# Kernel optimization log

Hardware: AMD Instinct MI355X
Metric: run time of the kernel (lower is better)

The kernel has to match this reference:

```python
import jax, jax.numpy as jnp
import numpy as np
from jax import lax

KS = 3          # kernel_size
ITER = 24       # diffusion iterations
# itertools.product([0,1,-1], repeat=2) order from the torch source
OFFS = [(i, j) for i in (0, 1, -1) for j in (0, 1, -1)]


def setup_inputs() -> dict:
    key = jax.random.key(0)
    k1, k2, k3 = jax.random.split(key, 3)
    B, H, W = 8, 512, 512
    x = jax.random.normal(k1, (B, 1, H, W), jnp.float32)
    W_aff = jax.random.normal(k2, (KS * KS - 1, 1, KS, KS), jnp.float32) * 0.1
    b_aff = jax.random.normal(k3, (KS * KS - 1,), jnp.float32) * 0.1
    return {"x": x, "W_aff": W_aff, "b_aff": b_aff}


def _gen_kernel(aff):
    # aff: [B, 8, H, W] -> normalized 9-channel kernel [B, 9, H, W]
    abs_sum = jnp.sum(jnp.abs(aff), axis=1, keepdims=True)
    a = aff / abs_sum
    s = jnp.sum(a, axis=1, keepdims=True)
    return jnp.concatenate([1.0 - s, a], axis=1)


def reference(x, W_aff, b_aff):
    # affinity net: 1 -> 8 channel 3x3 SAME conv
    aff = lax.conv_general_dilated(x, W_aff, (1, 1), "SAME") + b_aff[None, :, None, None]
    kernel = _gen_kernel(aff)  # [B, 9, H, W]
    H, W = x.shape[2], x.shape[3]

    def body(_, xc):
        # zero-pad then take 9 shifted views: col_k[p] = x[p - off_k] (zero outside)
        xp = jnp.pad(xc, ((0, 0), (0, 0), (1, 1), (1, 1)))
        cols = jnp.concatenate(
            [xp[:, :, 1 - oi:1 - oi + H, 1 - oj:1 - oj + W] for (oi, oj) in OFFS],
            axis=1,
        )  # [B, 9, H, W]
        return jnp.sum(cols * kernel, axis=1, keepdims=True)

    return lax.fori_loop(0, ITER, body, x)
```

## Files before the change

### kernel.cpp

```cpp
#include <hip/hip_runtime.h>
#include <hip/hip_fp16.h>

constexpr int B = 8, H = 512, W = 512;
constexpr int N = B * H * W;
constexpr int HW = H * W;

constexpr int TT = 32;
constexpr int T  = 6;
constexpr int XR = TT + 2 * T;
constexpr int XE = XR * XR;
constexpr int NG = XR / 4;
constexpr int CR = XR - 2;
constexpr int NGT = CR * NG;
constexpr int NTH = H / TT, NTW = W / TT;
constexpr int NTILES = B * NTH * NTW;
constexpr int NT = 512;
constexpr int NF2 = XR * (XR / 2);

__global__ __launch_bounds__(256) void cspn_gen_kernel(
    const float* __restrict__ x, const float* __restrict__ Wa,
    const float* __restrict__ ba, __half* __restrict__ Kh) {
  int idx = blockIdx.x * 256 + threadIdx.x;
  if (idx >= N) return;
  int j = idx & (W - 1);
  int i = (idx >> 9) & (H - 1);
  const float* xb = x + (idx & ~(HW - 1));

  float v[9];
#pragma unroll
  for (int u = 0; u < 3; ++u) {
#pragma unroll
    for (int t = 0; t < 3; ++t) {
      int ii = i + u - 1, jj = j + t - 1;
      v[u * 3 + t] = (unsigned(ii) < (unsigned)H && unsigned(jj) < (unsigned)W)
                         ? xb[ii * W + jj]
                         : 0.0f;
    }
  }

  float aff[8];
  float abs_sum = 0.0f;
#pragma unroll
  for (int c = 0; c < 8; ++c) {
    float a = ba[c];
#pragma unroll
    for (int t = 0; t < 9; ++t) a += v[t] * Wa[c * 9 + t];
    aff[c] = a;
    abs_sum += fabsf(a);
  }
  float inv = 1.0f / abs_sum;
#pragma unroll
  for (int c = 0; c < 8; ++c) aff[c] *= inv;

  union { uint4 u; __half2 h[4]; } pk;
#pragma unroll
  for (int c = 0; c < 4; ++c)
    pk.h[c] = __floats2half2_rn(aff[2 * c], aff[2 * c + 1]);
  *reinterpret_cast<uint4*>(Kh + (size_t)idx * 8) = pk.u;
}

#define H2F(h) __half2float(h)

__global__ __launch_bounds__(NT, 6) void cspn_fused(
    const float* __restrict__ xin, const __half* __restrict__ Kh,
    float* __restrict__ xout) {
  __shared__ __align__(16) float sBuf[64 + 2 * XE + 64];
  float* sX = sBuf + 64;

  int bid = blockIdx.x;
  int wg = (bid & 7) * (NTILES / 8) + (bid >> 3);
  int b  = wg / (NTH * NTW);
  int rr = wg % (NTH * NTW);
  int ti0 = (rr / NTW) * TT, tj0 = (rr % NTW) * TT;
  int tid = threadIdx.x;

  bool active = tid < NGT;
  int xi  = 1 + tid / NG;
  int xj0 = (tid % NG) * 4;

  const float* xb = xin + (size_t)b * HW;

  int li0 = tid / (XR / 2), gc0 = tid - li0 * (XR / 2);
  int p1 = tid + NT;
  int li1 = p1 / (XR / 2), gc1 = p1 - li1 * (XR / 2);
  bool st1 = p1 < NF2;
  float2 sv0 = make_float2(0.f, 0.f), sv1 = make_float2(0.f, 0.f);
  {
    int gi = ti0 + li0 - T, gj = tj0 + 2 * gc0 - T;
    if ((unsigned)gi < (unsigned)H && (unsigned)gj < (unsigned)W)
      sv0 = *reinterpret_cast<const float2*>(xb + gi * W + gj);
  }
  if (st1) {
    int gi = ti0 + li1 - T, gj = tj0 + 2 * gc1 - T;
    if ((unsigned)gi < (unsigned)H && (unsigned)gj < (unsigned)W)
      sv1 = *reinterpret_cast<const float2*>(xb + gi * W + gj);
  }

  __half2 kh[4][4];
  float4 k0;
  {
    int gi  = ti0 + xi - T;
    int gj0 = tj0 + xj0 - T;
    bool rowv = active && (unsigned)gi < (unsigned)H;
    const __half* Kb =
        Kh + ((size_t)b * HW + (size_t)(rowv ? gi : 0) * W) * 8;
    float k0v[4];
#pragma unroll
    for (int p = 0; p < 4; ++p) {
      int gj = gj0 + p;
      union { uint4 u; __half2 h[4]; } pk;
      pk.u = make_uint4(0u, 0u, 0u, 0u);
      if (rowv && (unsigned)gj < (unsigned)W)
        pk.u = *reinterpret_cast<const uint4*>(Kb + (size_t)gj * 8);
      float2 f01 = __half22float2(pk.h[0]);
      float2 f23 = __half22float2(pk.h[1]);
      float2 f45 = __half22float2(pk.h[2]);
      float2 f67 = __half22float2(pk.h[3]);
      k0v[p] = 1.0f - (f01.x + f01.y + f23.x + f23.y +
                       f45.x + f45.y + f67.x + f67.y);
      kh[p][0] = pk.h[0]; kh[p][1] = pk.h[1];
      kh[p][2] = pk.h[2]; kh[p][3] = pk.h[3];
    }
    k0 = make_float4(k0v[0], k0v[1], k0v[2], k0v[3]);
  }

  *reinterpret_cast<float2*>(sX + li0 * XR + 2 * gc0) = sv0;
  if (st1) *reinterpret_cast<float2*>(sX + li1 * XR + 2 * gc1) = sv1;
  if (tid < 64) {
    sBuf[tid] = 0.f;
    sBuf[64 + 2 * XE + tid] = 0.f;
  }
  if (tid < 2 * XR) {
    int r = (tid < XR) ? 0 : (XR - 1);
    int c = (tid < XR) ? tid : tid - XR;
    sX[XE + r * XR + c] = 0.f;
  }
  __syncthreads();

  int base = xi * XR + xj0;
  float4 c1;
  if (active) c1 = *reinterpret_cast<const float4*>(sX + base);
#pragma unroll
  for (int s = 0; s < T; ++s) {
    const float* Xc = sX + (s & 1) * XE;
    float* Xn = sX + (((s & 1) ^ 1)) * XE;
    if (active) {
      const float* eu = Xc + base - XR - 1;
      const float* ec = Xc + base - 1;
      const float* ed = Xc + base + XR - 1;
      float l0 = eu[0], r0 = eu[5];
      float l1 = ec[0], r1 = ec[5];
      float l2 = ed[0], r2 = ed[5];
      float4 c0 = *reinterpret_cast<const float4*>(eu + 1);
      float4 c2 = *reinterpret_cast<const float4*>(ed + 1);
      float4 acc;
      acc.x = k0.x * c1.x
            + H2F(kh[0][0].x) * l1   + H2F(kh[0][0].y) * c1.y
            + H2F(kh[0][1].x) * c0.x + H2F(kh[0][1].y) * l0
            + H2F(kh[0][2].x) * c0.y + H2F(kh[0][2].y) * c2.x
            + H2F(kh[0][3].x) * l2   + H2F(kh[0][3].y) * c2.y;
      acc.y = k0.y * c1.y
            + H2F(kh[1][0].x) * c1.x + H2F(kh[1][0].y) * c1.z
            + H2F(kh[1][1].x) * c0.y + H2F(kh[1][1].y) * c0.x
            + H2F(kh[1][2].x) * c0.z + H2F(kh[1][2].y) * c2.y
            + H2F(kh[1][3].x) * c2.x + H2F(kh[1][3].y) * c2.z;
      acc.z = k0.z * c1.z
            + H2F(kh[2][0].x) * c1.y + H2F(kh[2][0].y) * c1.w
            + H2F(kh[2][1].x) * c0.z + H2F(kh[2][1].y) * c0.y
            + H2F(kh[2][2].x) * c0.w + H2F(kh[2][2].y) * c2.z
            + H2F(kh[2][3].x) * c2.y + H2F(kh[2][3].y) * c2.w;
      acc.w = k0.w * c1.w
            + H2F(kh[3][0].x) * c1.z + H2F(kh[3][0].y) * r1
            + H2F(kh[3][1].x) * c0.w + H2F(kh[3][1].y) * c0.z
            + H2F(kh[3][2].x) * r0   + H2F(kh[3][2].y) * c2.w
            + H2F(kh[3][3].x) * c2.z + H2F(kh[3][3].y) * r2;
      *reinterpret_cast<float4*>(Xn + base) = acc;
      c1 = acc;
    }
    __syncthreads();
  }

  float* yb = xout + (size_t)b * HW;
  int i  = tid >> 4;
  int pj = (tid & 15) * 2;
  float2 v = *reinterpret_cast<const float2*>(sX + (i + T) * XR + (pj + T));
  *reinterpret_cast<float2*>(yb + (size_t)(ti0 + i) * W + (tj0 + pj)) = v;
}

extern "C" void kernel_launch(void* const* d_in, const int* in_sizes, int n_in,
                              void* d_out, int out_size, void* d_ws,
                              size_t ws_size, hipStream_t stream) {
  const float* x  = (const float*)d_in[0];
  const float* Wa = (const float*)d_in[1];
  const float* ba = (const float*)d_in[2];
  float* out = (float*)d_out;

  __half* Kh = (__half*)d_ws;
  float* xa = (float*)d_ws + 4 * (size_t)N;
  cspn_gen_kernel<<<dim3(N / 256), dim3(256), 0, stream>>>(x, Wa, ba, Kh);

  const float* src = x;
  for (int l = 0; l < 24 / T; ++l) {
    float* dst = (l & 1) ? out : xa;
    cspn_fused<<<dim3(NTILES), dim3(NT), 0, stream>>>(src, Kh, dst);
    src = dst;
  }
}
```

Baseline: 115.0 us.

## Fuse affinity kernel generation into diffusion kernel, recomputing per launch

Removes the separate kernel-generation pass and its fp16 workspace buffer. Each diffusion launch now recomputes the 3x3 affinity conv and normalization from the original input for its tile, keeping all 9 weights in fp32 registers. This trades the global write and re-read of the packed half kernel for redundant compute in each of the four launches. It also raises register pressure under the existing launch bounds, and the per-thread scalar global loads of x0 are uncoalesced.

```diff
diff --git a/kernel.cpp b/kernel.cpp
--- a/kernel.cpp
+++ b/kernel.cpp
@@ -1,5 +1,4 @@
 #include <hip/hip_runtime.h>
-#include <hip/hip_fp16.h>
 
 constexpr int B = 8, H = 512, W = 512;
 constexpr int N = B * H * W;
@@ -17,52 +16,9 @@
 constexpr int NT = 512;
 constexpr int NF2 = XR * (XR / 2);
 
-__global__ __launch_bounds__(256) void cspn_gen_kernel(
-    const float* __restrict__ x, const float* __restrict__ Wa,
-    const float* __restrict__ ba, __half* __restrict__ Kh) {
-  int idx = blockIdx.x * 256 + threadIdx.x;
-  if (idx >= N) return;
-  int j = idx & (W - 1);
-  int i = (idx >> 9) & (H - 1);
-  const float* xb = x + (idx & ~(HW - 1));
-
-  float v[9];
-#pragma unroll
-  for (int u = 0; u < 3; ++u) {
-#pragma unroll
-    for (int t = 0; t < 3; ++t) {
-      int ii = i + u - 1, jj = j + t - 1;
-      v[u * 3 + t] = (unsigned(ii) < (unsigned)H && unsigned(jj) < (unsigned)W)
-                         ? xb[ii * W + jj]
-                         : 0.0f;
-    }
-  }
-
-  float aff[8];
-  float abs_sum = 0.0f;
-#pragma unroll
-  for (int c = 0; c < 8; ++c) {
-    float a = ba[c];
-#pragma unroll
-    for (int t = 0; t < 9; ++t) a += v[t] * Wa[c * 9 + t];
-    aff[c] = a;
-    abs_sum += fabsf(a);
-  }
-  float inv = 1.0f / abs_sum;
-#pragma unroll
-  for (int c = 0; c < 8; ++c) aff[c] *= inv;
-
-  union { uint4 u; __half2 h[4]; } pk;
-#pragma unroll
-  for (int c = 0; c < 4; ++c)
-    pk.h[c] = __floats2half2_rn(aff[2 * c], aff[2 * c + 1]);
-  *reinterpret_cast<uint4*>(Kh + (size_t)idx * 8) = pk.u;
-}
-
-#define H2F(h) __half2float(h)
-
 __global__ __launch_bounds__(NT, 6) void cspn_fused(
-    const float* __restrict__ xin, const __half* __restrict__ Kh,
+    const float* __restrict__ x0, const float* __restrict__ Wa,
+    const float* __restrict__ ba, const float* __restrict__ xin,
     float* __restrict__ xout) {
   __shared__ __align__(16) float sBuf[64 + 2 * XE + 64];
   float* sX = sBuf + 64;
@@ -78,7 +34,8 @@
   int xi  = 1 + tid / NG;
   int xj0 = (tid % NG) * 4;
 
-  const float* xb = xin + (size_t)b * HW;
+  const float* xb  = xin + (size_t)b * HW;
+  const float* x0b = x0 + (size_t)b * HW;
 
   int li0 = tid / (XR / 2), gc0 = tid - li0 * (XR / 2);
   int p1 = tid + NT;
@@ -96,32 +53,49 @@
       sv1 = *reinterpret_cast<const float2*>(xb + gi * W + gj);
   }
 
-  __half2 kh[4][4];
-  float4 k0;
-  {
+  float kkv[9][4];
+  if (active) {
     int gi  = ti0 + xi - T;
     int gj0 = tj0 + xj0 - T;
-    bool rowv = active && (unsigned)gi < (unsigned)H;
-    const __half* Kb =
-        Kh + ((size_t)b * HW + (size_t)(rowv ? gi : 0) * W) * 8;
-    float k0v[4];
+    float rv[3][6];
+#pragma unroll
+    for (int r = 0; r < 3; ++r) {
+      int ii = gi - 1 + r;
+      bool rv_ok = (unsigned)ii < (unsigned)H;
+      const float* row = x0b + (size_t)(rv_ok ? ii : 0) * W;
+#pragma unroll
+      for (int q = 0; q < 6; ++q) {
+        int jj = gj0 - 1 + q;
+        rv[r][q] = (rv_ok && (unsigned)jj < (unsigned)W) ? row[jj] : 0.f;
+      }
+    }
 #pragma unroll
     for (int p = 0; p < 4; ++p) {
-      int gj = gj0 + p;
-      union { uint4 u; __half2 h[4]; } pk;
-      pk.u = make_uint4(0u, 0u, 0u, 0u);
-      if (rowv && (unsigned)gj < (unsigned)W)
-        pk.u = *reinterpret_cast<const uint4*>(Kb + (size_t)gj * 8);
-      float2 f01 = __half22float2(pk.h[0]);
-      float2 f23 = __half22float2(pk.h[1]);
-      float2 f45 = __half22float2(pk.h[2]);
-      float2 f67 = __half22float2(pk.h[3]);
-      k0v[p] = 1.0f - (f01.x + f01.y + f23.x + f23.y +
-                       f45.x + f45.y + f67.x + f67.y);
-      kh[p][0] = pk.h[0]; kh[p][1] = pk.h[1];
-      kh[p][2] = pk.h[2]; kh[p][3] = pk.h[3];
+      float aff[8];
+      float abs_sum = 0.f;
+#pragma unroll
+      for (int c = 0; c < 8; ++c) {
+        float a = ba[c];
+#pragma unroll
+        for (int u = 0; u < 3; ++u)
+#pragma unroll
+          for (int q = 0; q < 3; ++q)
+            a += rv[u][p + q] * Wa[c * 9 + u * 3 + q];
+        aff[c] = a;
+        abs_sum += fabsf(a);
+      }
+      float inv = 1.0f / abs_sum;
+      float s = 0.f;
+#pragma unroll
+      for (int c = 0; c < 8; ++c) {
+        aff[c] *= inv;
+        s += aff[c];
+      }
+      bool pxv = (unsigned)gi < (unsigned)H && (unsigned)(gj0 + p) < (unsigned)W;
+      kkv[0][p] = pxv ? (1.0f - s) : 1.0f;
+#pragma unroll
+      for (int c = 0; c < 8; ++c) kkv[c + 1][p] = pxv ? aff[c] : 0.f;
     }
-    k0 = make_float4(k0v[0], k0v[1], k0v[2], k0v[3]);
   }
 
   *reinterpret_cast<float2*>(sX + li0 * XR + 2 * gc0) = sv0;
@@ -146,34 +120,26 @@
     float* Xn = sX + (((s & 1) ^ 1)) * XE;
     if (active) {
       const float* eu = Xc + base - XR - 1;
+      const float* ed = Xc + base + XR - 1;
       const float* ec = Xc + base - 1;
-      const float* ed = Xc + base + XR - 1;
       float l0 = eu[0], r0 = eu[5];
       float l1 = ec[0], r1 = ec[5];
       float l2 = ed[0], r2 = ed[5];
       float4 c0 = *reinterpret_cast<const float4*>(eu + 1);
       float4 c2 = *reinterpret_cast<const float4*>(ed + 1);
       float4 acc;
-      acc.x = k0.x * c1.x
-            + H2F(kh[0][0].x) * l1   + H2F(kh[0][0].y) * c1.y
-            + H2F(kh[0][1].x) * c0.x + H2F(kh[0][1].y) * l0
-            + H2F(kh[0][2].x) * c0.y + H2F(kh[0][2].y) * c2.x
-            + H2F(kh[0][3].x) * l2   + H2F(kh[0][3].y) * c2.y;
-      acc.y = k0.y * c1.y
-            + H2F(kh[1][0].x) * c1.x + H2F(kh[1][0].y) * c1.z
-            + H2F(kh[1][1].x) * c0.y + H2F(kh[1][1].y) * c0.x
-            + H2F(kh[1][2].x) * c0.z + H2F(kh[1][2].y) * c2.y
-            + H2F(kh[1][3].x) * c2.x + H2F(kh[1][3].y) * c2.z;
-      acc.z = k0.z * c1.z
-            + H2F(kh[2][0].x) * c1.y + H2F(kh[2][0].y) * c1.w
-            + H2F(kh[2][1].x) * c0.z + H2F(kh[2][1].y) * c0.y
-            + H2F(kh[2][2].x) * c0.w + H2F(kh[2][2].y) * c2.z
-            + H2F(kh[2][3].x) * c2.y + H2F(kh[2][3].y) * c2.w;
-      acc.w = k0.w * c1.w
-            + H2F(kh[3][0].x) * c1.z + H2F(kh[3][0].y) * r1
-            + H2F(kh[3][1].x) * c0.w + H2F(kh[3][1].y) * c0.z
-            + H2F(kh[3][2].x) * r0   + H2F(kh[3][2].y) * c2.w
-            + H2F(kh[3][3].x) * c2.z + H2F(kh[3][3].y) * r2;
+      acc.x = kkv[0][0] * c1.x + kkv[1][0] * l1   + kkv[2][0] * c1.y
+            + kkv[3][0] * c0.x + kkv[4][0] * l0   + kkv[5][0] * c0.y
+            + kkv[6][0] * c2.x + kkv[7][0] * l2   + kkv[8][0] * c2.y;
+      acc.y = kkv[0][1] * c1.y + kkv[1][1] * c1.x + kkv[2][1] * c1.z
+            + kkv[3][1] * c0.y + kkv[4][1] * c0.x + kkv[5][1] * c0.z
+            + kkv[6][1] * c2.y + kkv[7][1] * c2.x + kkv[8][1] * c2.z;
+      acc.z = kkv[0][2] * c1.z + kkv[1][2] * c1.y + kkv[2][2] * c1.w
+            + kkv[3][2] * c0.z + kkv[4][2] * c0.y + kkv[5][2] * c0.w
+            + kkv[6][2] * c2.z + kkv[7][2] * c2.y + kkv[8][2] * c2.w;
+      acc.w = kkv[0][3] * c1.w + kkv[1][3] * c1.z + kkv[2][3] * r1
+            + kkv[3][3] * c0.w + kkv[4][3] * c0.z + kkv[5][3] * r0
+            + kkv[6][3] * c2.w + kkv[7][3] * c2.z + kkv[8][3] * r2;
       *reinterpret_cast<float4*>(Xn + base) = acc;
       c1 = acc;
     }
@@ -194,15 +160,12 @@
   const float* Wa = (const float*)d_in[1];
   const float* ba = (const float*)d_in[2];
   float* out = (float*)d_out;
-
-  __half* Kh = (__half*)d_ws;
-  float* xa = (float*)d_ws + 4 * (size_t)N;
-  cspn_gen_kernel<<<dim3(N / 256), dim3(256), 0, stream>>>(x, Wa, ba, Kh);
+  float* xa = (float*)d_ws;
 
   const float* src = x;
   for (int l = 0; l < 24 / T; ++l) {
     float* dst = (l & 1) ? out : xa;
-    cspn_fused<<<dim3(NTILES), dim3(NT), 0, stream>>>(src, Kh, dst);
+    cspn_fused<<<dim3(NTILES), dim3(NT), 0, stream>>>(x, Wa, ba, src, dst);
     src = dst;
   }
 }
```

Measured after the change: 144.5 us. 1.26x slower.
